# Kernel tuning notes

Hardware: AMD Instinct MI355X
Metric: run time of the kernel (lower is better)

The kernel has to match this reference:

```python
import jax, jax.numpy as jnp
import numpy as np

B, T, N, H, E, LH, OUT, D = 64, 12, 325, 64, 32, 128, 12, 1
META_OFF = 65  # x[..., :1] is the signal, x[..., 65:] is the 32-dim temporal meta input


def _mlp(meta, W1, b1, W2, b2):
    # meta: (B,E); W1: (4,E,LH); W2: (4,LH,O) -> (4,B,O); 4 = gates g,i,f,o
    h = jax.nn.relu(jnp.einsum('be,geh->gbh', meta, W1) + b1[:, None, :])
    return jnp.einsum('gbh,gho->gbo', h, W2) + b2[:, None, :]


def setup_inputs() -> dict:
    key = jax.random.key(0)
    ks = jax.random.split(key, 16)
    s = lambda k, shape: jax.random.normal(k, shape, dtype=jnp.float32) * 0.05
    return {
        'x': jax.random.normal(ks[0], (B, T, N, 1 + 64 + E), dtype=jnp.float32),
        'lwx_W1': s(ks[1], (4, E, LH)), 'lwx_b1': s(ks[2], (4, LH)),
        'lwx_W2': s(ks[3], (4, LH, D * H)), 'lwx_b2': s(ks[4], (4, D * H)),
        'lwh_W1': s(ks[5], (4, E, LH)), 'lwh_b1': s(ks[6], (4, LH)),
        'lwh_W2': s(ks[7], (4, LH, H * H)), 'lwh_b2': s(ks[8], (4, H * H)),
        'lb_W1': s(ks[9], (4, E, LH)), 'lb_b1': s(ks[10], (4, LH)),
        'lb_W2': s(ks[11], (4, LH, H)), 'lb_b2': s(ks[12], (4, H)),
        'fc1_W': s(ks[13], (H, H // 2)), 'fc1_b': jnp.zeros((H // 2,), jnp.float32),
        'fc2_W': s(ks[14], (H // 2, OUT * D)), 'fc2_b': jnp.zeros((OUT * D,), jnp.float32),
    }


def reference(x, lwx_W1, lwx_b1, lwx_W2, lwx_b2,
              lwh_W1, lwh_b1, lwh_W2, lwh_b2,
              lb_W1, lb_b1, lb_W2, lb_b2,
              fc1_W, fc1_b, fc2_W, fc2_b):
    batch = x.shape[0]
    meta = jnp.mean(x[:, :, 0, META_OFF:], axis=1)  # (B,E)
    xs = jnp.transpose(x[..., :D], (1, 0, 2, 3))    # (T,B,N,D)

    Wx = _mlp(meta, lwx_W1, lwx_b1, lwx_W2, lwx_b2).reshape(4, batch, D, H)
    Wh = _mlp(meta, lwh_W1, lwh_b1, lwh_W2, lwh_b2).reshape(4, batch, H, H)
    b = _mlp(meta, lb_W1, lb_b1, lb_W2, lb_b2).reshape(4, batch, 1, H)

    def step(carry, xt):
        h, c = carry
        # (4,B,N,H): per-batch weights -> batched matmuls for all 4 gates
        z = (jnp.einsum('bnd,gbdh->gbnh', xt, Wx)
             + jnp.einsum('bnh,gbhk->gbnk', h, Wh) + b)
        g = jnp.tanh(z[0])
        i = jax.nn.sigmoid(z[1])
        f = jax.nn.sigmoid(z[2])
        o = jax.nn.sigmoid(z[3])
        c = g * i + c * f
        h = jnp.tanh(c) * o
        return (h, c), None

    # h0=c0=0 reproduces the torch t==0 special case exactly
    h0 = jnp.zeros((batch, N, H), x.dtype)
    (h, _), _ = jax.lax.scan(step, (h0, h0), xs)

    out = jax.nn.relu(h)
    out = jax.nn.relu(out @ fc1_W + fc1_b) @ fc2_W + fc2_b  # (B,N,OUT*D)
    out = out.reshape(batch, N, OUT, D)
    return jnp.transpose(out, (0, 2, 1, 3))  # (B,OUT,N,D)
```

## Files before the change

### kernel.cpp

```cpp
#include <hip/hip_runtime.h>
#include <stdint.h>

#define TT 12
#define NN 325
#define HH 64
#define EE 32
#define LHH 128
#define OO 12
#define CIN 97
#define MOFF 65
#define BB 64

typedef __attribute__((ext_vector_type(8))) short bf8;
typedef __attribute__((ext_vector_type(4))) float f4;

__device__ __forceinline__ float sigf(float x) {
  return __builtin_amdgcn_rcpf(1.f + __builtin_amdgcn_exp2f(-1.4426950408889634f * x));
}
__device__ __forceinline__ float tanhfast(float x) {
  return 1.f - 2.f * __builtin_amdgcn_rcpf(1.f + __builtin_amdgcn_exp2f(2.8853900817779268f * x));
}
__device__ __forceinline__ unsigned short f2bf(float f) {
  unsigned int u = __float_as_uint(f);
  u += 0x7fffu + ((u >> 16) & 1u);
  return (unsigned short)(u >> 16);
}
__device__ __forceinline__ float bf2f(unsigned short s) {
  return __uint_as_float(((unsigned int)s) << 16);
}

__global__ __launch_bounds__(256) void k_meta(
    const float* __restrict__ x,
    const float* __restrict__ xw1, const float* __restrict__ xb1,
    const float* __restrict__ xw2, const float* __restrict__ xb2,
    const float* __restrict__ hw1, const float* __restrict__ hb1,
    const float* __restrict__ bw1, const float* __restrict__ bb1,
    const float* __restrict__ bw2, const float* __restrict__ bb2,
    float* __restrict__ hid_ws, float* __restrict__ wx_ws,
    float* __restrict__ bg_ws)
{
  const int b = blockIdx.x, tid = threadIdx.x;
  __shared__ float meta_s[EE];
  __shared__ float hidx_s[512], hidb_s[512];

  if (tid < EE) {
    float s = 0.f;
    #pragma unroll
    for (int t = 0; t < TT; ++t)
      s += x[(size_t)((b * TT + t) * NN) * CIN + MOFF + tid];
    meta_s[tid] = s * (1.f / 12.f);
  }
  __syncthreads();

  for (int idx = tid; idx < 1536; idx += 256) {
    const int mlp = idx >> 9, rem = idx & 511;
    const int g = rem >> 7, l = rem & 127;
    const float* W1 = (mlp == 0) ? xw1 : ((mlp == 1) ? hw1 : bw1);
    const float* B1 = (mlp == 0) ? xb1 : ((mlp == 1) ? hb1 : bb1);
    float a = B1[rem];
    const float* w = W1 + g * (EE * LHH) + l;
    #pragma unroll
    for (int e = 0; e < EE; ++e) a = fmaf(meta_s[e], w[e * LHH], a);
    a = fmaxf(a, 0.f);
    if (mlp == 0) hidx_s[rem] = a;
    else if (mlp == 2) hidb_s[rem] = a;
    else hid_ws[g * (BB * LHH) + b * LHH + l] = a;
  }
  __syncthreads();

  {
    const int g = tid >> 6;
    const int h = tid & 63;
    float ax = xb2[tid];
    float ab = bb2[tid];
    const float* wxp = xw2 + (size_t)g * (LHH * HH) + h;
    const float* wbp = bw2 + (size_t)g * (LHH * HH) + h;
    const float* hx = hidx_s + g * LHH;
    const float* hb = hidb_s + g * LHH;
    #pragma unroll 8
    for (int l = 0; l < LHH; ++l) {
      ax = fmaf(hx[l], wxp[l * HH], ax);
      ab = fmaf(hb[l], wbp[l * HH], ab);
    }
    wx_ws[b * 256 + tid] = ax;
    bg_ws[b * 256 + tid] = ab;
  }
}

__global__ __launch_bounds__(256) void k_wh(
    const float* __restrict__ x,
    const float* __restrict__ hw2, const float* __restrict__ hb2,
    const float* __restrict__ hid_ws, unsigned short* __restrict__ whb,
    float* __restrict__ xg)
{
  const int g = blockIdx.x >> 6, i = blockIdx.x & 63, tid = threadIdx.x;
  __shared__ float hs[BB][132];
  __shared__ float w2s[LHH][HH];

  {
    const int base = blockIdx.x * 976;
    #pragma unroll
    for (int kk = 0; kk < 4; ++kk) {
      const int flat = base + kk * 256 + tid;
      if (flat < BB * TT * NN) {
        const int b = flat / (TT * NN);
        const int r = flat - b * (TT * NN);
        const int t = r / NN;
        const int n = r - t * NN;
        xg[flat] = x[(size_t)((b * TT + t) * NN + n) * CIN];
      }
    }
  }

  for (int idx = tid; idx < BB * LHH; idx += 256)
    hs[idx >> 7][idx & 127] = hid_ws[g * (BB * LHH) + idx];
  for (int idx = tid; idx < LHH * HH; idx += 256)
    w2s[idx >> 6][idx & 63] = hw2[(size_t)(g * LHH + (idx >> 6)) * 4096 + i * 64 + (idx & 63)];
  __syncthreads();

  const int rg = tid >> 4, cg = tid & 15;
  const int b0 = rg * 4, j0 = cg * 4;
  float acc[4][4] = {};
  for (int l = 0; l < LHH; l += 4) {
    f4 hv[4];
    #pragma unroll
    for (int rr = 0; rr < 4; ++rr) hv[rr] = *(const f4*)&hs[b0 + rr][l];
    #pragma unroll
    for (int ll = 0; ll < 4; ++ll) {
      const f4 wv = *(const f4*)&w2s[l + ll][j0];
      #pragma unroll
      for (int rr = 0; rr < 4; ++rr)
        #pragma unroll
        for (int jj = 0; jj < 4; ++jj)
          acc[rr][jj] = fmaf(hv[rr][ll], wv[jj], acc[rr][jj]);
    }
  }

  const int kh = i >> 5, quad = (i >> 3) & 3, j8 = i & 7;
  #pragma unroll
  for (int rr = 0; rr < 4; ++rr) {
    const int b = b0 + rr;
    #pragma unroll
    for (int jj = 0; jj < 4; ++jj) {
      const int j = j0 + jj;
      const float v = acc[rr][jj] + hb2[g * 4096 + i * 64 + j];
      const int col = g * 64 + j;
      const int nt = col >> 4, c16 = col & 15;
      const int lane = quad * 16 + c16;
      whb[(size_t)((b * 32 + kh * 16 + nt) * 64 + lane) * 8 + j8] = f2bf(v);
    }
  }
}

__global__ __launch_bounds__(256, 4) void k_lstm(
    const float* __restrict__ xg, const float* __restrict__ wx_ws,
    const float* __restrict__ bg_ws, const unsigned short* __restrict__ whb,
    const float* __restrict__ fc1W, const float* __restrict__ fc1b,
    const float* __restrict__ fc2W, const float* __restrict__ fc2b,
    float* __restrict__ out)
{
  const int rb = blockIdx.x, b = blockIdx.y, tid = threadIdx.x;
  const int wave = tid >> 6, lane = tid & 63, quad = lane >> 4, c16 = lane & 15;
  const int n0 = rb * 16;

  __shared__ __align__(16) unsigned short Hs[2][16][72];
  __shared__ float Xs[TT][16];
  __shared__ float fc1s[HH * 32];
  __shared__ float fc2s[32 * OO];
  __shared__ float HIDs[16][34];
  __shared__ float fc1bs[32];
  __shared__ float fc2bs[OO];

  for (int idx = tid; idx < TT * 16; idx += 256) {
    const int t = idx >> 4, r = idx & 15, n = n0 + r;
    Xs[t][r] = (n < NN) ? xg[b * (TT * NN) + t * NN + n] : 0.f;
  }
  for (int idx = tid; idx < HH * 32; idx += 256) fc1s[idx] = fc1W[idx];
  for (int idx = tid; idx < 32 * OO; idx += 256) fc2s[idx] = fc2W[idx];
  if (tid < 32) fc1bs[tid] = fc1b[tid];
  if (tid < OO) fc2bs[tid] = fc2b[tid];

  float wxv[4], bgv[4];
  #pragma unroll
  for (int g = 0; g < 4; ++g) {
    wxv[g] = wx_ws[b * 256 + g * 64 + wave * 16 + c16];
    bgv[g] = bg_ws[b * 256 + g * 64 + wave * 16 + c16];
  }
  bf8 wf[2][4];
  #pragma unroll
  for (int kh = 0; kh < 2; ++kh)
    #pragma unroll
    for (int g = 0; g < 4; ++g)
      wf[kh][g] = *(const bf8*)(whb + (size_t)((b * 32 + kh * 16 + g * 4 + wave) * 64 + lane) * 8);

  float cst[4];
  #pragma unroll
  for (int r = 0; r < 4; ++r) cst[r] = 0.f;

  __syncthreads();

  #pragma unroll 1
  for (int t = 0; t < TT; ++t) {
    float xr[4];
    #pragma unroll
    for (int r = 0; r < 4; ++r) xr[r] = Xs[t][quad * 4 + r];

    bf8 af0, af1;
    if (t > 0) {
      af0 = *(const bf8*)&Hs[(t - 1) & 1][c16][quad * 8];
      af1 = *(const bf8*)&Hs[(t - 1) & 1][c16][32 + quad * 8];
    }

    f4 a0, a1, a2, a3;
    #pragma unroll
    for (int r = 0; r < 4; ++r) {
      a0[r] = fmaf(xr[r], wxv[0], bgv[0]);
      a1[r] = fmaf(xr[r], wxv[1], bgv[1]);
      a2[r] = fmaf(xr[r], wxv[2], bgv[2]);
      a3[r] = fmaf(xr[r], wxv[3], bgv[3]);
    }
    if (t > 0) {
      a0 = __builtin_amdgcn_mfma_f32_16x16x32_bf16(af0, wf[0][0], a0, 0, 0, 0);
      a0 = __builtin_amdgcn_mfma_f32_16x16x32_bf16(af1, wf[1][0], a0, 0, 0, 0);
      a1 = __builtin_amdgcn_mfma_f32_16x16x32_bf16(af0, wf[0][1], a1, 0, 0, 0);
      a1 = __builtin_amdgcn_mfma_f32_16x16x32_bf16(af1, wf[1][1], a1, 0, 0, 0);
      a2 = __builtin_amdgcn_mfma_f32_16x16x32_bf16(af0, wf[0][2], a2, 0, 0, 0);
      a2 = __builtin_amdgcn_mfma_f32_16x16x32_bf16(af1, wf[1][2], a2, 0, 0, 0);
      a3 = __builtin_amdgcn_mfma_f32_16x16x32_bf16(af0, wf[0][3], a3, 0, 0, 0);
      a3 = __builtin_amdgcn_mfma_f32_16x16x32_bf16(af1, wf[1][3], a3, 0, 0, 0);
    }
    #pragma unroll
    for (int r = 0; r < 4; ++r) {
      const float gg = tanhfast(a0[r]);
      const float ii = sigf(a1[r]);
      const float ff = sigf(a2[r]);
      const float oo = sigf(a3[r]);
      const float cc = fmaf(gg, ii, cst[r] * ff);
      cst[r] = cc;
      const float hh = tanhfast(cc) * oo;
      Hs[t & 1][quad * 4 + r][wave * 16 + c16] = f2bf(hh);
    }
    __syncthreads();
  }

  {
    const int row = tid & 15, uu = tid >> 4;
    float h0 = fc1bs[2 * uu], h1 = fc1bs[2 * uu + 1];
    #pragma unroll
    for (int kc = 0; kc < 8; ++kc) {
      const bf8 hv = *(const bf8*)&Hs[1][row][kc * 8];
      #pragma unroll
      for (int j = 0; j < 8; ++j) {
        const float hk = fmaxf(bf2f((unsigned short)hv[j]), 0.f);
        const int k = kc * 8 + j;
        h0 = fmaf(hk, fc1s[k * 32 + 2 * uu], h0);
        h1 = fmaf(hk, fc1s[k * 32 + 2 * uu + 1], h1);
      }
    }
    HIDs[row][2 * uu] = fmaxf(h0, 0.f);
    HIDs[row][2 * uu + 1] = fmaxf(h1, 0.f);
  }
  __syncthreads();
  if (tid < 16 * OO) {
    const int o = tid >> 4, row = tid & 15;
    float acc = fc2bs[o];
    #pragma unroll
    for (int k = 0; k < 32; ++k)
      acc = fmaf(HIDs[row][k], fc2s[k * OO + o], acc);
    const int n = n0 + row;
    if (n < NN)
      out[b * (OO * NN) + o * NN + n] = acc;
  }
}

extern "C" void kernel_launch(void* const* d_in, const int* in_sizes, int n_in,
                              void* d_out, int out_size, void* d_ws, size_t ws_size,
                              hipStream_t stream) {
  const float* x    = (const float*)d_in[0];
  const float* xw1  = (const float*)d_in[1];
  const float* xb1  = (const float*)d_in[2];
  const float* xw2  = (const float*)d_in[3];
  const float* xb2  = (const float*)d_in[4];
  const float* hw1  = (const float*)d_in[5];
  const float* hb1  = (const float*)d_in[6];
  const float* hw2  = (const float*)d_in[7];
  const float* hb2  = (const float*)d_in[8];
  const float* bw1  = (const float*)d_in[9];
  const float* bb1  = (const float*)d_in[10];
  const float* bw2  = (const float*)d_in[11];
  const float* bb2  = (const float*)d_in[12];
  const float* fc1W = (const float*)d_in[13];
  const float* fc1b = (const float*)d_in[14];
  const float* fc2W = (const float*)d_in[15];
  const float* fc2b = (const float*)d_in[16];
  float* out = (float*)d_out;

  float* ws = (float*)d_ws;
  float* hid_ws = ws;
  float* wx_ws  = ws + 32768;
  float* bg_ws  = ws + 49152;
  float* xg_ws  = ws + 65536;
  unsigned short* whb = (unsigned short*)(ws + 65536 + BB * TT * NN);

  k_meta<<<64, 256, 0, stream>>>(x, xw1, xb1, xw2, xb2, hw1, hb1, bw1, bb1,
                                 bw2, bb2, hid_ws, wx_ws, bg_ws);
  k_wh<<<256, 256, 0, stream>>>(x, hw2, hb2, hid_ws, whb, xg_ws);
  k_lstm<<<dim3(21, 64), 256, 0, stream>>>(xg_ws, wx_ws, bg_ws, whb,
                                           fc1W, fc1b, fc2W, fc2b, out);
}
```

Baseline: 224.9 us.

## Fuse meta and Wh prep kernels; process 32 nodes per LSTM block

Merges k_meta and k_wh into one k_prep kernel. Every block recomputes the meta means, 256 blocks each recompute the hidden layer of the Wh MLP for their gate, and 8 extra blocks build the Wx and bias gate vectors. This removes one launch and the hid_ws round trip at the cost of redundant first-layer work in every block. The LSTM kernel now handles two 16-row tiles per block (32 nodes), so the per-batch Wh fragments are reused across both tiles and the grid shrinks from 21 to 11 blocks in x. The price is more registers, with occupancy bounds lowered from 4 to 3.

New measurement: 247.0 us. +9.8%, slower.

```diff
diff --git a/kernel.cpp b/kernel.cpp
--- a/kernel.cpp
+++ b/kernel.cpp
@@ -29,76 +29,35 @@
   return __uint_as_float(((unsigned int)s) << 16);
 }
 
-__global__ __launch_bounds__(256) void k_meta(
+__global__ __launch_bounds__(256, 2) void k_prep(
     const float* __restrict__ x,
     const float* __restrict__ xw1, const float* __restrict__ xb1,
     const float* __restrict__ xw2, const float* __restrict__ xb2,
     const float* __restrict__ hw1, const float* __restrict__ hb1,
+    const float* __restrict__ hw2, const float* __restrict__ hb2,
     const float* __restrict__ bw1, const float* __restrict__ bb1,
     const float* __restrict__ bw2, const float* __restrict__ bb2,
-    float* __restrict__ hid_ws, float* __restrict__ wx_ws,
-    float* __restrict__ bg_ws)
+    unsigned short* __restrict__ whb, float* __restrict__ xg,
+    float* __restrict__ wx_ws, float* __restrict__ bg_ws)
 {
-  const int b = blockIdx.x, tid = threadIdx.x;
-  __shared__ float meta_s[EE];
-  __shared__ float hidx_s[512], hidb_s[512];
-
-  if (tid < EE) {
-    float s = 0.f;
-    #pragma unroll
-    for (int t = 0; t < TT; ++t)
-      s += x[(size_t)((b * TT + t) * NN) * CIN + MOFF + tid];
-    meta_s[tid] = s * (1.f / 12.f);
-  }
-  __syncthreads();
-
-  for (int idx = tid; idx < 1536; idx += 256) {
-    const int mlp = idx >> 9, rem = idx & 511;
-    const int g = rem >> 7, l = rem & 127;
-    const float* W1 = (mlp == 0) ? xw1 : ((mlp == 1) ? hw1 : bw1);
-    const float* B1 = (mlp == 0) ? xb1 : ((mlp == 1) ? hb1 : bb1);
-    float a = B1[rem];
-    const float* w = W1 + g * (EE * LHH) + l;
-    #pragma unroll
-    for (int e = 0; e < EE; ++e) a = fmaf(meta_s[e], w[e * LHH], a);
-    a = fmaxf(a, 0.f);
-    if (mlp == 0) hidx_s[rem] = a;
-    else if (mlp == 2) hidb_s[rem] = a;
-    else hid_ws[g * (BB * LHH) + b * LHH + l] = a;
-  }
-  __syncthreads();
-
-  {
-    const int g = tid >> 6;
-    const int h = tid & 63;
-    float ax = xb2[tid];
-    float ab = bb2[tid];
-    const float* wxp = xw2 + (size_t)g * (LHH * HH) + h;
-    const float* wbp = bw2 + (size_t)g * (LHH * HH) + h;
-    const float* hx = hidx_s + g * LHH;
-    const float* hb = hidb_s + g * LHH;
-    #pragma unroll 8
-    for (int l = 0; l < LHH; ++l) {
-      ax = fmaf(hx[l], wxp[l * HH], ax);
-      ab = fmaf(hb[l], wbp[l * HH], ab);
-    }
-    wx_ws[b * 256 + tid] = ax;
-    bg_ws[b * 256 + tid] = ab;
-  }
-}
-
-__global__ __launch_bounds__(256) void k_wh(
-    const float* __restrict__ x,
-    const float* __restrict__ hw2, const float* __restrict__ hb2,
-    const float* __restrict__ hid_ws, unsigned short* __restrict__ whb,
-    float* __restrict__ xg)
-{
-  const int g = blockIdx.x >> 6, i = blockIdx.x & 63, tid = threadIdx.x;
+  const int bi = blockIdx.x, tid = threadIdx.x;
+  __shared__ float meta_s[BB][EE];
   __shared__ float hs[BB][132];
   __shared__ float w2s[LHH][HH];
 
-  {
-    const int base = blockIdx.x * 976;
+  for (int m = tid; m < BB * EE; m += 256) {
+    const int b = m >> 5, e = m & 31;
+    float s = 0.f;
+    #pragma unroll
+    for (int t = 0; t < TT; ++t)
+      s += x[(size_t)((b * TT + t) * NN) * CIN + MOFF + e];
+    meta_s[b][e] = s * (1.f / 12.f);
+  }
+
+  if (bi < 256) {
+    const int g = bi >> 6, i = bi & 63;
+
+    const int base = bi * 976;
     #pragma unroll
     for (int kk = 0; kk < 4; ++kk) {
       const int flat = base + kk * 256 + tid;
@@ -110,49 +69,84 @@
         xg[flat] = x[(size_t)((b * TT + t) * NN + n) * CIN];
       }
     }
-  }
-
-  for (int idx = tid; idx < BB * LHH; idx += 256)
-    hs[idx >> 7][idx & 127] = hid_ws[g * (BB * LHH) + idx];
-  for (int idx = tid; idx < LHH * HH; idx += 256)
-    w2s[idx >> 6][idx & 63] = hw2[(size_t)(g * LHH + (idx >> 6)) * 4096 + i * 64 + (idx & 63)];
-  __syncthreads();
-
-  const int rg = tid >> 4, cg = tid & 15;
-  const int b0 = rg * 4, j0 = cg * 4;
-  float acc[4][4] = {};
-  for (int l = 0; l < LHH; l += 4) {
-    f4 hv[4];
-    #pragma unroll
-    for (int rr = 0; rr < 4; ++rr) hv[rr] = *(const f4*)&hs[b0 + rr][l];
-    #pragma unroll
-    for (int ll = 0; ll < 4; ++ll) {
-      const f4 wv = *(const f4*)&w2s[l + ll][j0];
-      #pragma unroll
-      for (int rr = 0; rr < 4; ++rr)
+    for (int idx = tid; idx < LHH * HH; idx += 256)
+      w2s[idx >> 6][idx & 63] = hw2[(size_t)(g * LHH + (idx >> 6)) * 4096 + i * 64 + (idx & 63)];
+    __syncthreads();
+
+    for (int m = tid; m < BB * LHH; m += 256) {
+      const int b = m >> 7, l = m & 127;
+      float a = hb1[g * LHH + l];
+      const float* w = hw1 + (size_t)g * (EE * LHH) + l;
+      #pragma unroll
+      for (int e = 0; e < EE; ++e) a = fmaf(meta_s[b][e], w[e * LHH], a);
+      hs[b][l] = fmaxf(a, 0.f);
+    }
+    __syncthreads();
+
+    const int rg = tid >> 4, cg = tid & 15;
+    const int b0 = rg * 4, j0 = cg * 4;
+    float acc[4][4] = {};
+    for (int l = 0; l < LHH; l += 4) {
+      f4 hv[4];
+      #pragma unroll
+      for (int rr = 0; rr < 4; ++rr) hv[rr] = *(const f4*)&hs[b0 + rr][l];
+      #pragma unroll
+      for (int ll = 0; ll < 4; ++ll) {
+        const f4 wv = *(const f4*)&w2s[l + ll][j0];
         #pragma unroll
-        for (int jj = 0; jj < 4; ++jj)
-          acc[rr][jj] = fmaf(hv[rr][ll], wv[jj], acc[rr][jj]);
-    }
-  }
-
-  const int kh = i >> 5, quad = (i >> 3) & 3, j8 = i & 7;
-  #pragma unroll
-  for (int rr = 0; rr < 4; ++rr) {
-    const int b = b0 + rr;
-    #pragma unroll
-    for (int jj = 0; jj < 4; ++jj) {
-      const int j = j0 + jj;
-      const float v = acc[rr][jj] + hb2[g * 4096 + i * 64 + j];
-      const int col = g * 64 + j;
-      const int nt = col >> 4, c16 = col & 15;
-      const int lane = quad * 16 + c16;
-      whb[(size_t)((b * 32 + kh * 16 + nt) * 64 + lane) * 8 + j8] = f2bf(v);
-    }
-  }
-}
-
-__global__ __launch_bounds__(256, 4) void k_lstm(
+        for (int rr = 0; rr < 4; ++rr)
+          #pragma unroll
+          for (int jj = 0; jj < 4; ++jj)
+            acc[rr][jj] = fmaf(hv[rr][ll], wv[jj], acc[rr][jj]);
+      }
+    }
+    const int kh = i >> 5, quad = (i >> 3) & 3, j8 = i & 7;
+    #pragma unroll
+    for (int rr = 0; rr < 4; ++rr) {
+      const int b = b0 + rr;
+      #pragma unroll
+      for (int jj = 0; jj < 4; ++jj) {
+        const int j = j0 + jj;
+        const float v = acc[rr][jj] + hb2[g * 4096 + i * 64 + j];
+        const int col = g * 64 + j;
+        const int nt = col >> 4, c16 = col & 15;
+        const int lane = quad * 16 + c16;
+        whb[(size_t)((b * 32 + kh * 16 + nt) * 64 + lane) * 8 + j8] = f2bf(v);
+      }
+    }
+  } else {
+    const int role = bi - 256;
+    const int g = role >> 1;
+    const int isb = role & 1;
+    const float* W1 = isb ? bw1 : xw1;
+    const float* B1 = isb ? bb1 : xb1;
+    const float* W2 = isb ? bw2 : xw2;
+    const float* B2 = isb ? bb2 : xb2;
+    float* dst = isb ? bg_ws : wx_ws;
+    __syncthreads();
+
+    for (int m = tid; m < BB * LHH; m += 256) {
+      const int b = m >> 7, l = m & 127;
+      float a = B1[g * LHH + l];
+      const float* w = W1 + (size_t)g * (EE * LHH) + l;
+      #pragma unroll
+      for (int e = 0; e < EE; ++e) a = fmaf(meta_s[b][e], w[e * LHH], a);
+      hs[b][l] = fmaxf(a, 0.f);
+    }
+    __syncthreads();
+
+    for (int m = tid; m < BB * HH; m += 256) {
+      const int b = m >> 6, h = m & 63;
+      float a = B2[g * HH + h];
+      const float* w = W2 + (size_t)g * (LHH * HH) + h;
+      #pragma unroll 8
+      for (int l = 0; l < LHH; ++l) a = fmaf(hs[b][l], w[l * HH], a);
+      dst[b * 256 + g * 64 + h] = a;
+    }
+  }
+}
+
+__global__ __launch_bounds__(256, 3) void k_lstm(
     const float* __restrict__ xg, const float* __restrict__ wx_ws,
     const float* __restrict__ bg_ws, const unsigned short* __restrict__ whb,
     const float* __restrict__ fc1W, const float* __restrict__ fc1b,
@@ -161,18 +155,18 @@
 {
   const int rb = blockIdx.x, b = blockIdx.y, tid = threadIdx.x;
   const int wave = tid >> 6, lane = tid & 63, quad = lane >> 4, c16 = lane & 15;
-  const int n0 = rb * 16;
-
-  __shared__ __align__(16) unsigned short Hs[2][16][72];
-  __shared__ float Xs[TT][16];
+  const int n0 = rb * 32;
+
+  __shared__ __align__(16) unsigned short Hs[2][2][16][72];
+  __shared__ float Xs[TT][32];
   __shared__ float fc1s[HH * 32];
   __shared__ float fc2s[32 * OO];
-  __shared__ float HIDs[16][34];
+  __shared__ float HIDs[32][36];
   __shared__ float fc1bs[32];
   __shared__ float fc2bs[OO];
 
-  for (int idx = tid; idx < TT * 16; idx += 256) {
-    const int t = idx >> 4, r = idx & 15, n = n0 + r;
+  for (int idx = tid; idx < TT * 32; idx += 256) {
+    const int t = idx >> 5, r = idx & 31, n = n0 + r;
     Xs[t][r] = (n < NN) ? xg[b * (TT * NN) + t * NN + n] : 0.f;
   }
   for (int idx = tid; idx < HH * 32; idx += 256) fc1s[idx] = fc1W[idx];
@@ -193,83 +187,93 @@
     for (int g = 0; g < 4; ++g)
       wf[kh][g] = *(const bf8*)(whb + (size_t)((b * 32 + kh * 16 + g * 4 + wave) * 64 + lane) * 8);
 
-  float cst[4];
+  float cst[2][4];
   #pragma unroll
-  for (int r = 0; r < 4; ++r) cst[r] = 0.f;
+  for (int ta = 0; ta < 2; ++ta)
+    #pragma unroll
+    for (int r = 0; r < 4; ++r) cst[ta][r] = 0.f;
 
   __syncthreads();
 
   #pragma unroll 1
   for (int t = 0; t < TT; ++t) {
-    float xr[4];
-    #pragma unroll
-    for (int r = 0; r < 4; ++r) xr[r] = Xs[t][quad * 4 + r];
-
-    bf8 af0, af1;
+    bf8 af[2][2];
     if (t > 0) {
-      af0 = *(const bf8*)&Hs[(t - 1) & 1][c16][quad * 8];
-      af1 = *(const bf8*)&Hs[(t - 1) & 1][c16][32 + quad * 8];
-    }
-
-    f4 a0, a1, a2, a3;
-    #pragma unroll
-    for (int r = 0; r < 4; ++r) {
-      a0[r] = fmaf(xr[r], wxv[0], bgv[0]);
-      a1[r] = fmaf(xr[r], wxv[1], bgv[1]);
-      a2[r] = fmaf(xr[r], wxv[2], bgv[2]);
-      a3[r] = fmaf(xr[r], wxv[3], bgv[3]);
+      #pragma unroll
+      for (int ta = 0; ta < 2; ++ta) {
+        af[ta][0] = *(const bf8*)&Hs[(t - 1) & 1][ta][c16][quad * 8];
+        af[ta][1] = *(const bf8*)&Hs[(t - 1) & 1][ta][c16][32 + quad * 8];
+      }
+    }
+    f4 ac[2][4];
+    #pragma unroll
+    for (int ta = 0; ta < 2; ++ta) {
+      float xr[4];
+      #pragma unroll
+      for (int r = 0; r < 4; ++r) xr[r] = Xs[t][ta * 16 + quad * 4 + r];
+      #pragma unroll
+      for (int g = 0; g < 4; ++g)
+        #pragma unroll
+        for (int r = 0; r < 4; ++r)
+          ac[ta][g][r] = fmaf(xr[r], wxv[g], bgv[g]);
     }
     if (t > 0) {
-      a0 = __builtin_amdgcn_mfma_f32_16x16x32_bf16(af0, wf[0][0], a0, 0, 0, 0);
-      a0 = __builtin_amdgcn_mfma_f32_16x16x32_bf16(af1, wf[1][0], a0, 0, 0, 0);
-      a1 = __builtin_amdgcn_mfma_f32_16x16x32_bf16(af0, wf[0][1], a1, 0, 0, 0);
-      a1 = __builtin_amdgcn_mfma_f32_16x16x32_bf16(af1, wf[1][1], a1, 0, 0, 0);
-      a2 = __builtin_amdgcn_mfma_f32_16x16x32_bf16(af0, wf[0][2], a2, 0, 0, 0);
-      a2 = __builtin_amdgcn_mfma_f32_16x16x32_bf16(af1, wf[1][2], a2, 0, 0, 0);
-      a3 = __builtin_amdgcn_mfma_f32_16x16x32_bf16(af0, wf[0][3], a3, 0, 0, 0);
-      a3 = __builtin_amdgcn_mfma_f32_16x16x32_bf16(af1, wf[1][3], a3, 0, 0, 0);
-    }
-    #pragma unroll
-    for (int r = 0; r < 4; ++r) {
-      const float gg = tanhfast(a0[r]);
-      const float ii = sigf(a1[r]);
-      const float ff = sigf(a2[r]);
-      const float oo = sigf(a3[r]);
-      const float cc = fmaf(gg, ii, cst[r] * ff);
-      cst[r] = cc;
-      const float hh = tanhfast(cc) * oo;
-      Hs[t & 1][quad * 4 + r][wave * 16 + c16] = f2bf(hh);
-    }
+      #pragma unroll
+      for (int ta = 0; ta < 2; ++ta)
+        #pragma unroll
+        for (int g = 0; g < 4; ++g) {
+          ac[ta][g] = __builtin_amdgcn_mfma_f32_16x16x32_bf16(af[ta][0], wf[0][g], ac[ta][g], 0, 0, 0);
+          ac[ta][g] = __builtin_amdgcn_mfma_f32_16x16x32_bf16(af[ta][1], wf[1][g], ac[ta][g], 0, 0, 0);
+        }
+    }
+    #pragma unroll
+    for (int ta = 0; ta < 2; ++ta)
+      #pragma unroll
+      for (int r = 0; r < 4; ++r) {
+        const float gg = tanhfast(ac[ta][0][r]);
+        const float ii = sigf(ac[ta][1][r]);
+        const float ff = sigf(ac[ta][2][r]);
+        const float oo = sigf(ac[ta][3][r]);
+        const float cc = fmaf(gg, ii, cst[ta][r] * ff);
+        cst[ta][r] = cc;
+        const float hh = tanhfast(cc) * oo;
+        Hs[t & 1][ta][quad * 4 + r][wave * 16 + c16] = f2bf(hh);
+      }
     __syncthreads();
   }
 
   {
-    const int row = tid & 15, uu = tid >> 4;
-    float h0 = fc1bs[2 * uu], h1 = fc1bs[2 * uu + 1];
+    const int row32 = tid & 31, uu = tid >> 5;
+    const int ta = row32 >> 4, row = row32 & 15;
+    float hacc[4];
+    #pragma unroll
+    for (int j = 0; j < 4; ++j) hacc[j] = fc1bs[uu * 4 + j];
     #pragma unroll
     for (int kc = 0; kc < 8; ++kc) {
-      const bf8 hv = *(const bf8*)&Hs[1][row][kc * 8];
-      #pragma unroll
-      for (int j = 0; j < 8; ++j) {
-        const float hk = fmaxf(bf2f((unsigned short)hv[j]), 0.f);
-        const int k = kc * 8 + j;
-        h0 = fmaf(hk, fc1s[k * 32 + 2 * uu], h0);
-        h1 = fmaf(hk, fc1s[k * 32 + 2 * uu + 1], h1);
-      }
-    }
-    HIDs[row][2 * uu] = fmaxf(h0, 0.f);
-    HIDs[row][2 * uu + 1] = fmaxf(h1, 0.f);
+      const bf8 hv = *(const bf8*)&Hs[1][ta][row][kc * 8];
+      #pragma unroll
+      for (int j8 = 0; j8 < 8; ++j8) {
+        const float hk = fmaxf(bf2f((unsigned short)hv[j8]), 0.f);
+        const int k = kc * 8 + j8;
+        #pragma unroll
+        for (int j = 0; j < 4; ++j)
+          hacc[j] = fmaf(hk, fc1s[k * 32 + uu * 4 + j], hacc[j]);
+      }
+    }
+    #pragma unroll
+    for (int j = 0; j < 4; ++j)
+      HIDs[row32][uu * 4 + j] = fmaxf(hacc[j], 0.f);
   }
   __syncthreads();
-  if (tid < 16 * OO) {
-    const int o = tid >> 4, row = tid & 15;
-    float acc = fc2bs[o];
+  for (int idx = tid; idx < 32 * OO; idx += 256) {
+    const int o = idx >> 5, row32 = idx & 31;
+    float a = fc2bs[o];
     #pragma unroll
     for (int k = 0; k < 32; ++k)
-      acc = fmaf(HIDs[row][k], fc2s[k * OO + o], acc);
-    const int n = n0 + row;
+      a = fmaf(HIDs[row32][k], fc2s[k * OO + o], a);
+    const int n = n0 + row32;
     if (n < NN)
-      out[b * (OO * NN) + o * NN + n] = acc;
+      out[b * (OO * NN) + o * NN + n] = a;
   }
 }
 
@@ -296,15 +300,13 @@
   float* out = (float*)d_out;
 
   float* ws = (float*)d_ws;
-  float* hid_ws = ws;
-  float* wx_ws  = ws + 32768;
-  float* bg_ws  = ws + 49152;
-  float* xg_ws  = ws + 65536;
-  unsigned short* whb = (unsigned short*)(ws + 65536 + BB * TT * NN);
-
-  k_meta<<<64, 256, 0, stream>>>(x, xw1, xb1, xw2, xb2, hw1, hb1, bw1, bb1,
-                                 bw2, bb2, hid_ws, wx_ws, bg_ws);
-  k_wh<<<256, 256, 0, stream>>>(x, hw2, hb2, hid_ws, whb, xg_ws);
-  k_lstm<<<dim3(21, 64), 256, 0, stream>>>(xg_ws, wx_ws, bg_ws, whb,
+  float* wx_ws = ws;
+  float* bg_ws = ws + 16384;
+  float* xg_ws = ws + 32768;
+  unsigned short* whb = (unsigned short*)(ws + 32768 + BB * TT * NN);
+
+  k_prep<<<264, 256, 0, stream>>>(x, xw1, xb1, xw2, xb2, hw1, hb1, hw2, hb2,
+                                  bw1, bb1, bw2, bb2, whb, xg_ws, wx_ws, bg_ws);
+  k_lstm<<<dim3(11, 64), 256, 0, stream>>>(xg_ws, wx_ws, bg_ws, whb,
                                            fc1W, fc1b, fc2W, fc2b, out);
 }
```
